# Kernel optimization log

Hardware: AMD Instinct MI355X
Metric: run time of the kernel (lower is better)

The kernel has to match this reference:

```python
import jax, jax.numpy as jnp
import numpy as np

N = 8192
D_IN = 512
D_HID = 1024
D_OUT = 512
N_NEIGHS = 16


def setup_inputs() -> dict:
    key = jax.random.key(0)
    k1, k2, k3 = jax.random.split(key, 3)
    x = jax.random.normal(k1, (N, D_IN), dtype=jnp.float32)
    # build a fake_edge_mask with exactly N_NEIGHS ones per row (distinct cols)
    rows = jnp.arange(N)[:, None]                      # [N,1]
    cols = (rows + 1 + jnp.arange(N_NEIGHS)[None, :]) % N  # [N,K] distinct
    fake_edge_mask = jnp.zeros((N, N), dtype=jnp.bool_).at[rows, cols].set(True)
    real_edge_mask = jnp.zeros((N, N), dtype=jnp.bool_)  # unused by forward math
    W1 = jax.random.normal(k2, (D_IN, D_HID), dtype=jnp.float32) * (1.0 / np.sqrt(D_IN))
    b1 = jnp.zeros((D_HID,), dtype=jnp.float32)
    W2 = jax.random.normal(k3, (D_HID, D_OUT), dtype=jnp.float32) * (1.0 / np.sqrt(D_HID))
    b2 = jnp.zeros((D_OUT,), dtype=jnp.float32)
    return {"x": x, "real_edge_mask": real_edge_mask, "fake_edge_mask": fake_edge_mask,
            "W1": W1, "b1": b1, "W2": W2, "b2": b2}


def reference(x, real_edge_mask, fake_edge_mask, W1, b1, W2, b2):
    # torch.nonzero(mask)[:,1].reshape(N, K): per-row column indices of the K ones.
    # top_k on 0/1 values returns the K ones' indices (tie-break = ascending index);
    # the subsequent sum is permutation-invariant so ordering is irrelevant.
    _, idx = jax.lax.top_k(fake_edge_mask.astype(jnp.float32), N_NEIGHS)  # [N,K]
    niche_feat = x[idx]                                  # [N,K,D] gather
    res = jnp.sum(niche_feat, axis=1) / N_NEIGHS         # mean over neighbors
    hidden = x + res                                     # residual add
    h = jax.nn.relu(hidden @ W1 + b1)                    # fc1 + ReLU
    out = h @ W2 + b2                                    # fc2
    return out
```

## Files before the change

kernel.cpp:

```cpp
#include <hip/hip_runtime.h>

typedef __attribute__((ext_vector_type(8))) short sh8;
typedef __attribute__((ext_vector_type(4))) float fl4;

__device__ __forceinline__ unsigned short f2bf(float f) {
    unsigned int u = __float_as_uint(f);
    unsigned int r = (u + 0x7fffu + ((u >> 16) & 1u)) >> 16;
    return (unsigned short)r;
}

#define NROWS   8192
#define D_IN    512
#define D_HID   1024
#define D_OUT   512
#define NNEIGH  16

__global__ __launch_bounds__(256) void neigh_hidden(
    const float* __restrict__ x,
    const int* __restrict__ mask_w,
    unsigned short* __restrict__ hB)
{
    const int row = blockIdx.x;
    const int tid = threadIdx.x;
    __shared__ int idxs[64];
    __shared__ int ok_s;

    const bool i32mode = (mask_w[1] == 1);

    if (tid < 64) idxs[tid] = row;
    if (tid == 0) ok_s = 1;
    __syncthreads();

    if (tid < NNEIGH) {
        int c = row + 1 + tid; if (c >= NROWS) c -= NROWS;
        int set;
        if (i32mode) set = (mask_w[(size_t)row * NROWS + c] != 0);
        else         set = (((const unsigned char*)mask_w)[(size_t)row * NROWS + c] != 0);
        if (set) idxs[tid] = c;
        else     atomicAnd(&ok_s, 0);
    }
    __syncthreads();

    if (!ok_s) {
        __shared__ int cnt;
        if (tid == 0) cnt = 0;
        __syncthreads();
        for (int j = 0; j < NROWS / 256; j++) {
            int c = tid * (NROWS / 256) + j;
            int set = i32mode ? (mask_w[(size_t)row * NROWS + c] != 0)
                              : (((const unsigned char*)mask_w)[(size_t)row * NROWS + c] != 0);
            if (set) { int q = atomicAdd(&cnt, 1); if (q < 64) idxs[q] = c; }
        }
        __syncthreads();
    }

    float s0 = 0.f, s1 = 0.f;
    #pragma unroll 4
    for (int k = 0; k < NNEIGH; k++) {
        int idx = idxs[k];
        idx = (idx < 0) ? 0 : ((idx > NROWS - 1) ? NROWS - 1 : idx);
        const float2 v = ((const float2*)(x + (size_t)idx * D_IN))[tid];
        s0 += v.x; s1 += v.y;
    }
    const float2 xv = ((const float2*)(x + (size_t)row * D_IN))[tid];
    float h0 = xv.x + s0 * (1.f / 16.f);
    float h1 = xv.y + s1 * (1.f / 16.f);
    ushort2 o;
    o.x = f2bf(h0); o.y = f2bf(h1);
    *((ushort2*)(hB + (size_t)row * D_IN) + tid) = o;
}

__global__ __launch_bounds__(256) void transpose_cast(
    const float* __restrict__ in, unsigned short* __restrict__ out, int R, int C)
{
    __shared__ float tile[32][33];
    const int tx = threadIdx.x & 31, ty = threadIdx.x >> 5;
    const int c0 = blockIdx.x * 32, r0 = blockIdx.y * 32;
    #pragma unroll
    for (int k = 0; k < 4; k++)
        tile[ty + 8 * k][tx] = in[(size_t)(r0 + ty + 8 * k) * C + c0 + tx];
    __syncthreads();
    #pragma unroll
    for (int k = 0; k < 4; k++)
        out[(size_t)(c0 + ty + 8 * k) * R + r0 + tx] = f2bf(tile[tx][ty + 8 * k]);
}

template<bool RELU, bool OUT_BF16>
__global__ __launch_bounds__(256) void gemm_bt(
    const unsigned short* __restrict__ A,
    const unsigned short* __restrict__ Bt,
    const float* __restrict__ bias,
    void* __restrict__ Cout,
    int M, int N, int K)
{
    constexpr int LDT = 40;
    __shared__ unsigned short As[128 * LDT];
    __shared__ unsigned short Bs[128 * LDT];

    const int tid  = threadIdx.x;
    const long m0  = (long)blockIdx.y * 128;
    const long n0  = (long)blockIdx.x * 128;
    const int wave = tid >> 6, lane = tid & 63;
    const int wm = (wave >> 1) * 64, wn = (wave & 1) * 64;
    const int lm = lane & 15, k0 = (lane >> 4) * 8;

    fl4 acc[4][4] = {};

    for (int kt = 0; kt < K; kt += 32) {
        #pragma unroll
        for (int r = 0; r < 2; r++) {
            int L   = tid + r * 256;
            int row = L >> 2;
            int kv  = (L & 3) * 8;
            *(sh8*)(&As[row * LDT + kv]) = *(const sh8*)(&A [(m0 + row) * K + kt + kv]);
            *(sh8*)(&Bs[row * LDT + kv]) = *(const sh8*)(&Bt[(n0 + row) * K + kt + kv]);
        }
        __syncthreads();

        sh8 af[4], bf_[4];
        #pragma unroll
        for (int t = 0; t < 4; t++) {
            af[t]  = *(const sh8*)(&As[(wm + t * 16 + lm) * LDT + k0]);
            bf_[t] = *(const sh8*)(&Bs[(wn + t * 16 + lm) * LDT + k0]);
        }
        #pragma unroll
        for (int tm = 0; tm < 4; tm++)
            #pragma unroll
            for (int tn = 0; tn < 4; tn++)
                acc[tm][tn] = __builtin_amdgcn_mfma_f32_16x16x32_bf16(
                    af[tm], bf_[tn], acc[tm][tn], 0, 0, 0);
        __syncthreads();
    }

    const int rq = (lane >> 4) * 4;
    #pragma unroll
    for (int tm = 0; tm < 4; tm++) {
        #pragma unroll
        for (int tn = 0; tn < 4; tn++) {
            const long col = n0 + wn + tn * 16 + lm;
            const float bv = bias[col];
            #pragma unroll
            for (int r = 0; r < 4; r++) {
                const long row = m0 + wm + tm * 16 + rq + r;
                float v = acc[tm][tn][r] + bv;
                if (RELU) v = fmaxf(v, 0.f);
                if (OUT_BF16) ((unsigned short*)Cout)[row * N + col] = f2bf(v);
                else          ((float*)Cout)[row * N + col] = v;
            }
        }
    }
}

extern "C" void kernel_launch(void* const* d_in, const int* in_sizes, int n_in,
                              void* d_out, int out_size, void* d_ws, size_t ws_size,
                              hipStream_t stream)
{
    const float* x     = (const float*)d_in[0];
    const int*   fmask = (const int*)d_in[2];
    const float* W1    = (const float*)d_in[3];
    const float* b1    = (const float*)d_in[4];
    const float* W2    = (const float*)d_in[5];
    const float* b2    = (const float*)d_in[6];
    float*       out   = (float*)d_out;

    const size_t needElts = (size_t)NROWS * D_IN + (size_t)D_HID * D_IN
                          + (size_t)D_OUT * D_HID + (size_t)NROWS * D_HID;
    unsigned short* base = (ws_size >= needElts * sizeof(unsigned short))
                         ? (unsigned short*)d_ws
                         : (unsigned short*)d_in[1];

    unsigned short* hiddenB = base;
    unsigned short* W1t     = hiddenB + (size_t)NROWS * D_IN;
    unsigned short* W2t     = W1t + (size_t)D_HID * D_IN;
    unsigned short* h       = W2t + (size_t)D_OUT * D_HID;

    neigh_hidden<<<NROWS, 256, 0, stream>>>(x, fmask, hiddenB);
    transpose_cast<<<dim3(D_HID / 32, D_IN / 32), 256, 0, stream>>>(W1, W1t, D_IN, D_HID);
    transpose_cast<<<dim3(D_OUT / 32, D_HID / 32), 256, 0, stream>>>(W2, W2t, D_HID, D_OUT);
    gemm_bt<true,  true ><<<dim3(D_HID / 128, NROWS / 128), 256, 0, stream>>>(
        hiddenB, W1t, b1, h, NROWS, D_HID, D_IN);
    gemm_bt<false, false><<<dim3(D_OUT / 128, NROWS / 128), 256, 0, stream>>>(
        h, W2t, b2, out, NROWS, D_OUT, D_HID);
}
```

Before: 483.3 us.

## Load GEMM tiles directly into LDS with XOR swizzle and K-tile of 64

The bf16 GEMM now stages A and B tiles with global_load_lds 16-byte direct-to-LDS loads instead of going through registers. The K tile doubles from 32 to 64, giving two MFMA sub-steps per barrier pair. LDS padding is replaced by an XOR swizzle, applied on the global address side, to avoid bank conflicts. The aim is to cut VGPR staging traffic and halve the number of barriers, at the cost of more LDS per block and depending on gfx950 direct-load support.

```diff
diff --git a/kernel.cpp b/kernel.cpp
--- a/kernel.cpp
+++ b/kernel.cpp
@@ -8,6 +8,10 @@
     unsigned int r = (u + 0x7fffu + ((u >> 16) & 1u)) >> 16;
     return (unsigned short)r;
 }
+
+#define GLDS16(gp, lp) __builtin_amdgcn_global_load_lds( \
+    (const __attribute__((address_space(1))) void*)(gp), \
+    (__attribute__((address_space(3))) void*)(lp), 16, 0, 0)
 
 #define NROWS   8192
 #define D_IN    512
@@ -63,10 +67,9 @@
         s0 += v.x; s1 += v.y;
     }
     const float2 xv = ((const float2*)(x + (size_t)row * D_IN))[tid];
-    float h0 = xv.x + s0 * (1.f / 16.f);
-    float h1 = xv.y + s1 * (1.f / 16.f);
     ushort2 o;
-    o.x = f2bf(h0); o.y = f2bf(h1);
+    o.x = f2bf(xv.x + s0 * (1.f / 16.f));
+    o.y = f2bf(xv.y + s1 * (1.f / 16.f));
     *((ushort2*)(hB + (size_t)row * D_IN) + tid) = o;
 }
 
@@ -93,42 +96,53 @@
     void* __restrict__ Cout,
     int M, int N, int K)
 {
-    constexpr int LDT = 40;
-    __shared__ unsigned short As[128 * LDT];
-    __shared__ unsigned short Bs[128 * LDT];
+    __shared__ unsigned short As[128 * 64];
+    __shared__ unsigned short Bs[128 * 64];
 
     const int tid  = threadIdx.x;
     const long m0  = (long)blockIdx.y * 128;
     const long n0  = (long)blockIdx.x * 128;
     const int wave = tid >> 6, lane = tid & 63;
     const int wm = (wave >> 1) * 64, wn = (wave & 1) * 64;
-    const int lm = lane & 15, k0 = (lane >> 4) * 8;
+    const int lm = lane & 15, q8 = (lane >> 4) * 8;
+
+    int srow[4], skv[4];
+    #pragma unroll
+    for (int s = 0; s < 4; s++) {
+        const int L = tid * 8 + s * 2048;
+        srow[s] = L >> 6;
+        skv[s]  = (L & 63) ^ ((srow[s] & 7) << 3);
+    }
 
     fl4 acc[4][4] = {};
 
-    for (int kt = 0; kt < K; kt += 32) {
+    for (int kt = 0; kt < K; kt += 64) {
         #pragma unroll
-        for (int r = 0; r < 2; r++) {
-            int L   = tid + r * 256;
-            int row = L >> 2;
-            int kv  = (L & 3) * 8;
-            *(sh8*)(&As[row * LDT + kv]) = *(const sh8*)(&A [(m0 + row) * K + kt + kv]);
-            *(sh8*)(&Bs[row * LDT + kv]) = *(const sh8*)(&Bt[(n0 + row) * K + kt + kv]);
+        for (int s = 0; s < 4; s++) {
+            const int L = tid * 8 + s * 2048;
+            GLDS16(&A [(m0 + srow[s]) * K + kt + skv[s]], &As[L]);
+            GLDS16(&Bt[(n0 + srow[s]) * K + kt + skv[s]], &Bs[L]);
         }
         __syncthreads();
 
-        sh8 af[4], bf_[4];
         #pragma unroll
-        for (int t = 0; t < 4; t++) {
-            af[t]  = *(const sh8*)(&As[(wm + t * 16 + lm) * LDT + k0]);
-            bf_[t] = *(const sh8*)(&Bs[(wn + t * 16 + lm) * LDT + k0]);
+        for (int ks = 0; ks < 2; ks++) {
+            const int klog = ks * 32 + q8;
+            sh8 af[4], bf_[4];
+            #pragma unroll
+            for (int t = 0; t < 4; t++) {
+                const int ra = wm + t * 16 + lm;
+                const int rb = wn + t * 16 + lm;
+                af[t]  = *(const sh8*)(&As[ra * 64 + (klog ^ ((ra & 7) << 3))]);
+                bf_[t] = *(const sh8*)(&Bs[rb * 64 + (klog ^ ((rb & 7) << 3))]);
+            }
+            #pragma unroll
+            for (int tm = 0; tm < 4; tm++)
+                #pragma unroll
+                for (int tn = 0; tn < 4; tn++)
+                    acc[tm][tn] = __builtin_amdgcn_mfma_f32_16x16x32_bf16(
+                        af[tm], bf_[tn], acc[tm][tn], 0, 0, 0);
         }
-        #pragma unroll
-        for (int tm = 0; tm < 4; tm++)
-            #pragma unroll
-            for (int tn = 0; tn < 4; tn++)
-                acc[tm][tn] = __builtin_amdgcn_mfma_f32_16x16x32_bf16(
-                    af[tm], bf_[tn], acc[tm][tn], 0, 0, 0);
         __syncthreads();
     }
 
```

New measurement: 472.9 us. 2.2% less time.
